# Kernel optimization log

Hardware: AMD Instinct MI355X
Metric: run time of the kernel (lower is better)

## Reference

```python
import jax, jax.numpy as jnp
import numpy as np

B, C, H, W = 32, 384, 32, 32
NCH = 4           # chunks per branch (mixing_size = [4,4,4])
CH = C // NCH     # 96 channels per chunk


def setup_inputs() -> dict:
    key = jax.random.key(0)
    ks = iter(jax.random.split(key, 32))
    r = lambda shape, s=0.05: jax.random.normal(next(ks), shape, dtype=jnp.float32) * s
    inp = {"x": jax.random.normal(next(ks), (B, C, H, W), dtype=jnp.float32)}
    for b, k in zip((1, 2, 3), (1, 3, 5)):
        inp[f"f{b}_mlp_w1"] = r((2, CH, CH // 8))
        inp[f"f{b}_mlp_b1"] = r((2, CH // 8))
        inp[f"f{b}_mlp_w2"] = r((2, CH // 8, CH))
        inp[f"f{b}_mlp_b2"] = r((2, CH))
        inp[f"f{b}_conv_w"] = r((2, CH, 1, k, k))
        inp[f"f{b}_conv_b"] = r((2, CH))
    inp["fusion_w1"] = r((C, C // 4))
    inp["fusion_b1"] = r((C // 4,))
    inp["fusion_w2"] = r((C // 4, 3 * C))
    inp["fusion_b2"] = r((3 * C,))
    inp["proj_w"] = r((C, C))
    inp["proj_b"] = r((C,))
    return inp


def _gelu(x):
    return jax.nn.gelu(x, approximate=False)  # torch nn.GELU default (erf)


def _branch(x, mw1, mb1, mw2, mb2, cw, cb, pad):
    # x: (B, C, H, W); chunks of CH channels; even idx -> MLP (channel-last), odd -> depthwise conv
    chunks = jnp.split(x, NCH, axis=1)
    outs, mi, ci = [], 0, 0
    for i, c in enumerate(chunks):
        if i % 2 == 0:
            h = _gelu(jnp.einsum('bchw,cd->bdhw', c, mw1[mi]) + mb1[mi][:, None, None])
            y = jnp.einsum('bdhw,dc->bchw', h, mw2[mi]) + mb2[mi][:, None, None]
            mi += 1
        else:
            y = jax.lax.conv_general_dilated(
                c, cw[ci], window_strides=(1, 1), padding=[(pad, pad), (pad, pad)],
                feature_group_count=CH, dimension_numbers=('NCHW', 'OIHW', 'NCHW'))
            y = y + cb[ci][:, None, None]
            ci += 1
        outs.append(y)
    return jnp.concatenate(outs, axis=1)


def reference(x,
              f1_mlp_w1, f1_mlp_b1, f1_mlp_w2, f1_mlp_b2, f1_conv_w, f1_conv_b,
              f2_mlp_w1, f2_mlp_b1, f2_mlp_w2, f2_mlp_b2, f2_conv_w, f2_conv_b,
              f3_mlp_w1, f3_mlp_b1, f3_mlp_w2, f3_mlp_b2, f3_conv_w, f3_conv_b,
              fusion_w1, fusion_b1, fusion_w2, fusion_b2, proj_w, proj_b):
    x1 = _branch(x, f1_mlp_w1, f1_mlp_b1, f1_mlp_w2, f1_mlp_b2, f1_conv_w, f1_conv_b, pad=0)
    x2 = _branch(x, f2_mlp_w1, f2_mlp_b1, f2_mlp_w2, f2_mlp_b2, f2_conv_w, f2_conv_b, pad=1)
    x3 = _branch(x, f3_mlp_w1, f3_mlp_b1, f3_mlp_w2, f3_mlp_b2, f3_conv_w, f3_conv_b, pad=2)
    # softmax-gated multi-scale fusion
    a = (x1 + x2 + x3).mean(axis=(2, 3))                            # (B, C)
    g = _gelu(a @ fusion_w1 + fusion_b1) @ fusion_w2 + fusion_b2     # (B, 3C)
    g = g.reshape(a.shape[0], C, 3).transpose(2, 0, 1)               # (3, B, C)
    w = jax.nn.softmax(g, axis=0)[:, :, :, None, None]               # (3, B, C, 1, 1)
    comb = x1 * w[0] + x2 * w[1] + x3 * w[2]                         # (B, C, H, W)
    out = jnp.einsum('bchw,cd->bdhw', comb, proj_w) + proj_b[:, None, None]
    return out
```

## Files before the change

kernel.cpp:

```cpp
#include <hip/hip_runtime.h>
#include <math.h>

#define B_  32
#define C_  384
#define HW  1024

typedef float          f32x4 __attribute__((ext_vector_type(4)));
typedef short          s16x8 __attribute__((ext_vector_type(8)));
typedef unsigned short us8v  __attribute__((ext_vector_type(8)));

#define SWZ(pix) ((((pix) ^ ((pix) >> 4)) & 15) << 4)

struct KParams {
  const float* x;
  const float* mw1[3]; const float* mb1[3]; const float* mw2[3]; const float* mb2[3];
  const float* cw[3];  const float* cb[3];
  const float* fw1; const float* fb1; const float* fw2; const float* fb2;
  const float* pw;  const float* pb;
  float* wg;
  float* H_part;
  float* cvS;
  float* ext;
  unsigned short* pwT;
  unsigned short* hl;
  float* out;
};

__device__ __forceinline__ float gelu_exact(float v) {
  return 0.5f * v * (1.0f + erff(v * 0.70710678118654752440f));
}
__device__ __forceinline__ unsigned short f2bf(float f) {
  unsigned u = __float_as_uint(f);
  u += 0x7FFFu + ((u >> 16) & 1u);
  return (unsigned short)(u >> 16);
}
__device__ __forceinline__ float bf2f(unsigned short h) {
  return __uint_as_float(((unsigned)h) << 16);
}

template<int HALF>
__device__ __forceinline__ void conv_strip(const float* xc, int h0, int row,
                                           float w1t, const float* w3, const float* w5,
                                           float* y0, float* y1, float* y2) {
#pragma unroll
  for (int p = 0; p < 16; ++p) { y0[p] = 0.f; y1[p] = 0.f; y2[p] = 0.f; }
#pragma unroll
  for (int dy = 0; dy < 5; ++dy) {
    const int hr = h0 + row - 2 + dy;
    float win[20];
    if (hr >= 0 && hr < 32) {
#pragma unroll
      for (int u = 0; u < 5; ++u)
        *(float4*)&win[u*4] = *(const float4*)&xc[hr*32 + HALF*12 + u*4];
    } else {
#pragma unroll
      for (int u = 0; u < 20; ++u) win[u] = 0.f;
    }
#pragma unroll
    for (int dx = 0; dx < 5; ++dx) {
      const float w = w5[dy*5 + dx];
#pragma unroll
      for (int p = 0; p < 16; ++p) {
        const int ri = p + dx - 2 + HALF*4;
        if (ri >= 0 && ri < 20) y2[p] += win[ri] * w;
      }
    }
    if (dy >= 1 && dy <= 3) {
#pragma unroll
      for (int dx = 0; dx < 3; ++dx) {
        const float w = w3[(dy-1)*3 + dx];
#pragma unroll
        for (int p = 0; p < 16; ++p) {
          const int ri = p + dx - 1 + HALF*4;
          if (ri >= 0 && ri < 20) y1[p] += win[ri] * w;
        }
      }
      if (dy == 2) {
#pragma unroll
        for (int p = 0; p < 16; ++p) y0[p] = win[p + HALF*4] * w1t;
      }
    }
  }
}

__global__ __launch_bounds__(256, 2) void k_work(KParams P) {
  __shared__ __align__(16) char sm[49152 + 13824 + 256];
  const int bid = blockIdx.x;
  const int t = threadIdx.x;

  if (bid >= 1024) {
    const int pbk = bid - 1024;
    float (*tile)[33] = (float(*)[33])sm;
    const int td = pbk % 12, tc = pbk / 12;
    const int j = t & 31, i0 = t >> 5;
    const int gcoff = (tc < 3) ? 0 : (tc < 6 ? 96 : (tc < 9 ? -96 : 0));
    for (int i = i0; i < 32; i += 8)
      tile[i][j] = P.pw[(size_t)(tc*32 + i + gcoff)*C_ + td*32 + j];
    __syncthreads();
    for (int i = i0; i < 32; i += 8)
      P.pwT[(size_t)(td*32 + i)*C_ + tc*32 + j] = f2bf(tile[j][i]);
    return;
  }

  const int b = bid >> 5, sub = bid & 31;
  if (sub < 16) {
    const int mi = sub >> 3, q = sub & 7;
    const int h0 = q * 4;
    float* Xl  = (float*)sm;
    float* w1l = (float*)(sm + 49152);
    float* Hl  = (float*)(sm + 49152 + 13824);
    for (int i = t; i < 3456; i += 256) {
      int s = i / 1152, r = i - s*1152;
      w1l[i] = P.mw1[s][mi*1152 + r];
    }
    for (int i = t*4; i < 12288; i += 1024) {
      int c = i >> 7, pix = i & 127;
      *(float4*)&Xl[i] = *(const float4*)&P.x[(size_t)(b*C_ + mi*192 + c)*HW + h0*32 + pix];
    }
    __syncthreads();
    const int quad = t & 31, sjg = t >> 6;
    const int cq = (t >> 5) & 1;
    const int sj0 = sjg * 9;
    float h[9][4];
#pragma unroll
    for (int u = 0; u < 9; ++u) { h[u][0]=0.f; h[u][1]=0.f; h[u][2]=0.f; h[u][3]=0.f; }
    int wbase[9];
#pragma unroll
    for (int u = 0; u < 9; ++u) {
      int sj = sj0 + u, s = sj / 12, jj = sj % 12;
      wbase[u] = s*1152 + jj;
    }
    for (int c = cq*48; c < cq*48 + 48; ++c) {
      const float4 xv = *(const float4*)&Xl[c*128 + quad*4];
#pragma unroll
      for (int u = 0; u < 9; ++u) {
        const float w = w1l[wbase[u] + c*12];
        h[u][0] += xv.x*w; h[u][1] += xv.y*w; h[u][2] += xv.z*w; h[u][3] += xv.w*w;
      }
    }
#pragma unroll
    for (int u = 0; u < 9; ++u)
#pragma unroll
      for (int p = 0; p < 4; ++p) h[u][p] += __shfl_xor(h[u][p], 32, 64);
    float hs[9];
#pragma unroll
    for (int u = 0; u < 9; ++u) {
      int sj = sj0 + u, s = sj / 12, jj = sj % 12;
      const float bias = P.mb1[s][mi*12 + jj];
      float g[4];
#pragma unroll
      for (int p = 0; p < 4; ++p) g[p] = gelu_exact(h[u][p] + bias);
      if ((t & 63) < 32) {
        uint2 pk;
        pk.x = (unsigned)f2bf(g[0]) | ((unsigned)f2bf(g[1]) << 16);
        pk.y = (unsigned)f2bf(g[2]) | ((unsigned)f2bf(g[3]) << 16);
        *(uint2*)(P.hl + ((size_t)(b*2 + mi)*36 + sj)*1024 + q*128 + quad*4) = pk;
      }
      float sum = g[0] + g[1] + g[2] + g[3];
#pragma unroll
      for (int m = 16; m >= 1; m >>= 1) sum += __shfl_xor(sum, m, 64);
      hs[u] = sum;
    }
    if ((t & 63) == 0) {
#pragma unroll
      for (int u = 0; u < 9; ++u) Hl[sj0 + u] = hs[u];
    }
    __syncthreads();
    if (t < 36) P.H_part[(size_t)((b*2 + mi)*8 + q)*36 + t] = Hl[t];
  } else {
    const int s2 = sub - 16;
    const int gi = s2 >> 3, q = s2 & 7;
    const int h0 = q * 4;
    const int lane = t & 63, wv = t >> 6;
    const int gcbase = (2*gi + 1) * 96;
    for (int i = 0; i < 24; ++i) {
      const int cc = wv*24 + i;
      const float* xc = P.x + (size_t)(b*C_ + gcbase + cc)*HW + h0*32;
      const float2 v = *(const float2*)(xc + 2*lane);
      const float t2 = v.x + v.y;
      float T = t2;
      T += __shfl_xor(T, 1, 64);  T += __shfl_xor(T, 2, 64);
      T += __shfl_xor(T, 4, 64);  T += __shfl_xor(T, 8, 64);
      T += __shfl_xor(T, 16, 64); T += __shfl_xor(T, 32, 64);
      float c0  = ((lane & 15) == 0)  ? v.x : 0.f;
      float c1  = ((lane & 15) == 0)  ? v.y : 0.f;
      float c30 = ((lane & 15) == 15) ? v.x : 0.f;
      float c31 = ((lane & 15) == 15) ? v.y : 0.f;
      c0  += __shfl_xor(c0, 16, 64);  c0  += __shfl_xor(c0, 32, 64);
      c1  += __shfl_xor(c1, 16, 64);  c1  += __shfl_xor(c1, 32, 64);
      c30 += __shfl_xor(c30, 16, 64); c30 += __shfl_xor(c30, 32, 64);
      c31 += __shfl_xor(c31, 16, 64); c31 += __shfl_xor(c31, 32, 64);
      if (lane == 0) {
        float* S = &P.cvS[(((size_t)(b*2 + gi)*8 + q)*5)*96 + cc];
        S[0*96] = T;   S[1*96] = c0;  S[2*96] = c1;
        S[3*96] = c30; S[4*96] = c31;
      }
      if (q == 0 || q == 7) {
        float r = t2;
        r += __shfl_xor(r, 1, 64); r += __shfl_xor(r, 2, 64);
        r += __shfl_xor(r, 4, 64); r += __shfl_xor(r, 8, 64);
        const int e  = (q == 0) ? 0 : 1;
        const int lo = (q == 0) ? 0 : 32;
        const float Ra  = __shfl(r,   lo,      64), Rb  = __shfl(r,   lo + 16, 64);
        const float p00 = __shfl(v.x, lo,      64), p01 = __shfl(v.y, lo,      64);
        const float p0a = __shfl(v.x, lo + 15, 64), p0b = __shfl(v.y, lo + 15, 64);
        const float p10 = __shfl(v.x, lo + 16, 64), p11 = __shfl(v.y, lo + 16, 64);
        const float p1a = __shfl(v.x, lo + 31, 64), p1b = __shfl(v.y, lo + 31, 64);
        if (lane == 0) {
          float* E = &P.ext[((size_t)(b*2 + gi)*2 + e)*10*96 + cc];
          E[0*96] = Ra;  E[1*96] = Rb;
          E[2*96] = p00; E[3*96] = p01; E[4*96] = p0a; E[5*96] = p0b;
          E[6*96] = p10; E[7*96] = p11; E[8*96] = p1a; E[9*96] = p1b;
        }
      }
    }
  }
}

__global__ __launch_bounds__(512) void k_gate(KParams P) {
  const int b = blockIdx.x, t = threadIdx.x;
  __shared__ float am[C_], g1p[4][96], g1v[96], Hs[2][36];
  for (int i = t; i < 72; i += 512) {
    int mi = i / 36, sj = i % 36;
    float s = 0.f;
    for (int q = 0; q < 8; ++q) s += P.H_part[(size_t)((b*2+mi)*8 + q)*36 + sj];
    Hs[mi][sj] = s * (1.0f/1024.0f);
  }
  __syncthreads();
  if (t < 192) {
    const int mi = t / 96, cc = t % 96;
    float a = 0.f;
    for (int s = 0; s < 3; ++s) {
      float y = P.mb2[s][mi*96 + cc];
      for (int jj = 0; jj < 12; ++jj) y += Hs[mi][s*12+jj] * P.mw2[s][mi*1152 + jj*96 + cc];
      a += y;
    }
    am[mi*192 + cc] = a;
  } else if (t < 384) {
    const int i = t - 192;
    const int gi = i / 96, cc = i % 96;
    const float* S0 = &P.cvS[(((size_t)(b*2 + gi)*8)*5)*96 + cc];
    float T = 0.f, C0 = 0.f, C1 = 0.f, C30 = 0.f, C31 = 0.f;
#pragma unroll
    for (int q = 0; q < 8; ++q) {
      const float* Sq = S0 + (size_t)q*5*96;
      T += Sq[0*96]; C0 += Sq[1*96]; C1 += Sq[2*96]; C30 += Sq[3*96]; C31 += Sq[4*96];
    }
    const float* E0 = &P.ext[((size_t)(b*2 + gi)*2 + 0)*10*96 + cc];
    const float* E1 = &P.ext[((size_t)(b*2 + gi)*2 + 1)*10*96 + cc];
    const float R0  = E0[0*96], R1  = E0[1*96];
    const float a00 = E0[2*96], a01 = E0[3*96], a0a = E0[4*96], a0b = E0[5*96];
    const float a10 = E0[6*96], a11 = E0[7*96], a1a = E0[8*96], a1b = E0[9*96];
    const float R30 = E1[0*96], R31 = E1[1*96];
    const float b00 = E1[2*96], b01 = E1[3*96], b0a = E1[4*96], b0b = E1[5*96];
    const float b10 = E1[6*96], b11 = E1[7*96], b1a = E1[8*96], b1b = E1[9*96];
    const float ER[5]   = {R30+R31, R31, 0.f, R0, R0+R1};
    const float EC[5]   = {C30+C31, C31, 0.f, C0, C0+C1};
    const float cr0[5]  = {a0a+a0b, a0b, 0.f, a00, a00+a01};
    const float cr1[5]  = {a1a+a1b, a1b, 0.f, a10, a10+a11};
    const float cr30[5] = {b0a+b0b, b0b, 0.f, b00, b00+b01};
    const float cr31[5] = {b1a+b1b, b1b, 0.f, b10, b10+b11};
    const int gcl = gi*96 + cc;
    float sum = P.cw[0][gcl] * T;
#pragma unroll
    for (int dy = 0; dy < 3; ++dy)
#pragma unroll
      for (int dx = 0; dx < 3; ++dx) {
        const int s = dy - 1, u = dx - 1;
        float xc_ = 0.f;
        if (s == 1)  xc_ = cr0[u+2];
        if (s == -1) xc_ = cr31[u+2];
        sum += P.cw[1][gcl*9 + dy*3 + dx] * (T - ER[s+2] - EC[u+2] + xc_);
      }
#pragma unroll
    for (int dy = 0; dy < 5; ++dy)
#pragma unroll
      for (int dx = 0; dx < 5; ++dx) {
        const int s = dy - 2, u = dx - 2;
        float xc_ = 0.f;
        if (s == 1)  xc_ = cr0[u+2];
        if (s == 2)  xc_ = cr0[u+2] + cr1[u+2];
        if (s == -1) xc_ = cr31[u+2];
        if (s == -2) xc_ = cr30[u+2] + cr31[u+2];
        sum += P.cw[2][gcl*25 + dy*5 + dx] * (T - ER[s+2] - EC[u+2] + xc_);
      }
    am[(2*gi+1)*96 + cc] = sum * (1.0f/1024.0f)
                         + P.cb[0][gcl] + P.cb[1][gcl] + P.cb[2][gcl];
  }
  __syncthreads();
  if (t < 384) {
    const int quarter = t / 96, jj = t % 96;
    float acc = 0.f;
    for (int c = quarter*96; c < quarter*96 + 96; ++c) acc += am[c] * P.fw1[c*96 + jj];
    g1p[quarter][jj] = acc;
  }
  __syncthreads();
  if (t < 96) g1v[t] = gelu_exact(g1p[0][t] + g1p[1][t] + g1p[2][t] + g1p[3][t] + P.fb1[t]);
  __syncthreads();
  if (t < 384) {
    const int c = t;
    float l0 = P.fb2[c*3+0], l1 = P.fb2[c*3+1], l2 = P.fb2[c*3+2];
    for (int jj = 0; jj < 96; ++jj) {
      const float g = g1v[jj];
      const float* f = P.fw2 + jj*1152 + c*3;
      l0 += g*f[0]; l1 += g*f[1]; l2 += g*f[2];
    }
    const float m = fmaxf(l0, fmaxf(l1, l2));
    const float e0 = expf(l0-m), e1 = expf(l1-m), e2 = expf(l2-m);
    const float inv = 1.0f/(e0+e1+e2);
    P.wg[0*(B_*C_) + b*C_ + c] = e0*inv;
    P.wg[1*(B_*C_) + b*C_ + c] = e1*inv;
    P.wg[2*(B_*C_) + b*C_ + c] = e2*inv;
  }
}

__global__ __launch_bounds__(512, 1) void k_proj(KParams P) {
  __shared__ __align__(16) char smem[135168];
  char* combB = smem;
  char* hlB   = smem + 98304;
  unsigned short* wlB = (unsigned short*)(smem + 117120);
  float* wgl  = (float*)(smem + 130944);

  const int t  = threadIdx.x;
  const int rb = (blockIdx.x & 7) * 32 + (blockIdx.x >> 3);
  const int b  = rb >> 3;
  const int qv = rb & 7;
  const int h0 = qv * 4;

  for (int i = t; i < 1152; i += 512)
    wgl[i] = P.wg[(size_t)(i/C_)*(B_*C_) + b*C_ + (i % C_)];
  for (int i = t; i < 6912; i += 512) {
    int s = i / 2304, r = i - s*2304;
    wlB[i] = f2bf(P.mw2[s][r]);
  }
  for (int i = t; i < 2304; i += 512) {
    const int sjmi = i >> 5, pg = i & 31;
    const uint2 v = *(const uint2*)(P.hl + ((size_t)(b*72 + sjmi))*1024 + qv*128 + pg*4);
    *(uint2*)(hlB + sjmi*256 + pg*8) = v;
  }
  __syncthreads();

  for (int it = 0; it < 3; ++it) {
    const int tt = t + 512*it;
    const int hlf = (tt >= 768) ? 1 : 0;
    const int rem = tt - hlf*768;
    const int row = rem & 3, c192 = rem >> 2;
    const int gi = c192 / 96, cc = c192 - gi*96;
    const int gcl = gi*96 + cc;
    const int gc = (2*gi + 1)*96 + cc;
    const int kp = 192 + gi*96 + cc;
    const float* xc = P.x + (size_t)(b*C_ + gc)*HW;
    const float w1t = P.cw[0][gcl];
    float w3[9], w5[25];
#pragma unroll
    for (int k2 = 0; k2 < 9; ++k2)  w3[k2] = P.cw[1][gcl*9 + k2];
#pragma unroll
    for (int k2 = 0; k2 < 25; ++k2) w5[k2] = P.cw[2][gcl*25 + k2];
    float y0[16], y1[16], y2[16];
    if (hlf == 0) conv_strip<0>(xc, h0, row, w1t, w3, w5, y0, y1, y2);
    else          conv_strip<1>(xc, h0, row, w1t, w3, w5, y0, y1, y2);
    const float g0 = wgl[0*C_ + gc], g1 = wgl[1*C_ + gc], g2 = wgl[2*C_ + gc];
    const float cbg = g0*P.cb[0][gcl] + g1*P.cb[1][gcl] + g2*P.cb[2][gcl];
#pragma unroll
    for (int p = 0; p < 16; ++p) {
      const float v = g0*y0[p] + g1*y1[p] + g2*y2[p] + cbg;
      const int pix = row*32 + hlf*16 + p;
      const int off = pix*768 + ((kp*2) ^ SWZ(pix));
      *(unsigned short*)(combB + off) = f2bf(v);
    }
  }

  {
    const int ct = t & 15, pt = (t >> 4) & 15, mi = t >> 8;
    const int c0 = ct*6, pix0 = pt*8;
    float wgc[3][6];
#pragma unroll
    for (int s = 0; s < 3; ++s)
#pragma unroll
      for (int i = 0; i < 6; ++i) wgc[s][i] = wgl[s*C_ + mi*192 + c0 + i];
    float acc[6][8];
#pragma unroll
    for (int i = 0; i < 6; ++i) {
      float ai = 0.f;
#pragma unroll
      for (int s = 0; s < 3; ++s) ai += wgc[s][i] * P.mb2[s][mi*96 + c0 + i];
#pragma unroll
      for (int p = 0; p < 8; ++p) acc[i][p] = ai;
    }
#pragma unroll
    for (int s = 0; s < 3; ++s)
#pragma unroll
      for (int jj = 0; jj < 12; ++jj) {
        const us8v hv = *(const us8v*)(hlB + (mi*36 + s*12 + jj)*256 + pix0*2);
        float hf[8];
#pragma unroll
        for (int p = 0; p < 8; ++p) hf[p] = bf2f(hv[p]);
        const unsigned short* wp = wlB + (s*2 + mi)*1152 + jj*96 + c0;
        float gw[6];
#pragma unroll
        for (int i = 0; i < 6; ++i) gw[i] = bf2f(wp[i]) * wgc[s][i];
#pragma unroll
        for (int i = 0; i < 6; ++i)
#pragma unroll
          for (int p = 0; p < 8; ++p) acc[i][p] += gw[i]*hf[p];
      }
#pragma unroll
    for (int i = 0; i < 6; ++i)
#pragma unroll
      for (int p = 0; p < 8; ++p) {
        const int pix = pix0 + p;
        const int kp2 = mi*96 + c0 + i;
        const int off = pix*768 + ((kp2*2) ^ SWZ(pix));
        *(unsigned short*)(combB + off) = f2bf(acc[i][p]);
      }
  }
  __syncthreads();

  {
    const int lane = t & 63, wv = t >> 6;
    const int wm = wv & 1, wn = wv >> 1;
    const int l15 = lane & 15, l4 = lane >> 4;
    f32x4 acc[4][6];
#pragma unroll
    for (int mt = 0; mt < 4; ++mt)
#pragma unroll
      for (int nt = 0; nt < 6; ++nt) acc[mt][nt] = (f32x4){0.f,0.f,0.f,0.f};
    const char* pwTb = (const char*)P.pwT;
#pragma unroll 2
    for (int ks = 0; ks < 12; ++ks) {
      const int k0 = ks*32 + l4*8;
      s16x8 af[4], bfr[6];
#pragma unroll
      for (int mt = 0; mt < 4; ++mt) {
        const int m = wm*64 + mt*16 + l15;
        af[mt] = *(const s16x8*)(combB + m*768 + ((2*k0) ^ SWZ(m)));
      }
#pragma unroll
      for (int nt = 0; nt < 6; ++nt) {
        const int d = wn*96 + nt*16 + l15;
        bfr[nt] = *(const s16x8*)(pwTb + (size_t)d*768 + 2*k0);
      }
#pragma unroll
      for (int mt = 0; mt < 4; ++mt)
#pragma unroll
        for (int nt = 0; nt < 6; ++nt)
          acc[mt][nt] = __builtin_amdgcn_mfma_f32_16x16x32_bf16(af[mt], bfr[nt], acc[mt][nt], 0, 0, 0);
    }
#pragma unroll
    for (int nt = 0; nt < 6; ++nt) {
      const int d = wn*96 + nt*16 + l15;
      const float pbv = P.pb[d];
#pragma unroll
      for (int mt = 0; mt < 4; ++mt) {
        const int pix = wm*64 + mt*16 + l4*4;
        float4 o;
        o.x = acc[mt][nt][0] + pbv;
        o.y = acc[mt][nt][1] + pbv;
        o.z = acc[mt][nt][2] + pbv;
        o.w = acc[mt][nt][3] + pbv;
        *(float4*)&P.out[(size_t)(b*C_ + d)*HW + (h0 + (pix >> 5))*32 + (pix & 31)] = o;
      }
    }
  }
}

extern "C" void kernel_launch(void* const* d_in, const int* in_sizes, int n_in,
                              void* d_out, int out_size, void* d_ws, size_t ws_size,
                              hipStream_t stream) {
  KParams P;
  P.x = (const float*)d_in[0];
  for (int s = 0; s < 3; ++s) {
    const int base = 1 + s * 6;
    P.mw1[s] = (const float*)d_in[base + 0];
    P.mb1[s] = (const float*)d_in[base + 1];
    P.mw2[s] = (const float*)d_in[base + 2];
    P.mb2[s] = (const float*)d_in[base + 3];
    P.cw[s]  = (const float*)d_in[base + 4];
    P.cb[s]  = (const float*)d_in[base + 5];
  }
  P.fw1 = (const float*)d_in[19]; P.fb1 = (const float*)d_in[20];
  P.fw2 = (const float*)d_in[21]; P.fb2 = (const float*)d_in[22];
  P.pw  = (const float*)d_in[23]; P.pb  = (const float*)d_in[24];
  float* w = (float*)d_ws;
  P.wg     = w;
  P.H_part = w + 36864;
  P.cvS    = w + 55296;
  P.ext    = w + 301056;
  P.pwT    = (unsigned short*)(w + 423936);
  P.hl     = (unsigned short*)(w + 497664);
  P.out = (float*)d_out;

  k_work<<<1168, 256, 0, stream>>>(P);
  k_gate<<<32, 512, 0, stream>>>(P);
  k_proj<<<256, 512, 0, stream>>>(P);
}
```

Before: 248.2 us.

## Split work kernel into MLP and aux kernels; halve proj tile rows

The fused k_work kernel becomes two kernels. k_mlp handles the first-layer MLP blocks, and k_aux handles the conv-statistics and proj-weight transpose blocks, so the small blocks no longer reserve the large shared-memory footprint. k_proj now processes 2 image rows per block instead of 4, which doubles the grid to 512 blocks and cuts shared memory from about 132KB to 75KB. The intent is better occupancy and more parallelism in the dominant kernel. The cost is an extra launch, and each proj-weight fragment is reused across fewer pixel rows, so loads of pwT from global/L2 double.

```diff
diff --git a/kernel.cpp b/kernel.cpp
--- a/kernel.cpp
+++ b/kernel.cpp
@@ -83,14 +83,82 @@
   }
 }
 
-__global__ __launch_bounds__(256, 2) void k_work(KParams P) {
+__global__ __launch_bounds__(256, 2) void k_mlp(KParams P) {
   __shared__ __align__(16) char sm[49152 + 13824 + 256];
   const int bid = blockIdx.x;
   const int t = threadIdx.x;
-
-  if (bid >= 1024) {
-    const int pbk = bid - 1024;
-    float (*tile)[33] = (float(*)[33])sm;
+  const int b = bid >> 4, mi = (bid >> 3) & 1, q = bid & 7;
+  const int h0 = q * 4;
+  float* Xl  = (float*)sm;
+  float* w1l = (float*)(sm + 49152);
+  float* Hl  = (float*)(sm + 49152 + 13824);
+  for (int i = t; i < 3456; i += 256) {
+    int s = i / 1152, r = i - s*1152;
+    w1l[i] = P.mw1[s][mi*1152 + r];
+  }
+  for (int i = t*4; i < 12288; i += 1024) {
+    int c = i >> 7, pix = i & 127;
+    *(float4*)&Xl[i] = *(const float4*)&P.x[(size_t)(b*C_ + mi*192 + c)*HW + h0*32 + pix];
+  }
+  __syncthreads();
+  const int quad = t & 31, sjg = t >> 6;
+  const int cq = (t >> 5) & 1;
+  const int sj0 = sjg * 9;
+  float h[9][4];
+#pragma unroll
+  for (int u = 0; u < 9; ++u) { h[u][0]=0.f; h[u][1]=0.f; h[u][2]=0.f; h[u][3]=0.f; }
+  int wbase[9];
+#pragma unroll
+  for (int u = 0; u < 9; ++u) {
+    int sj = sj0 + u, s = sj / 12, jj = sj % 12;
+    wbase[u] = s*1152 + jj;
+  }
+  for (int c = cq*48; c < cq*48 + 48; ++c) {
+    const float4 xv = *(const float4*)&Xl[c*128 + quad*4];
+#pragma unroll
+    for (int u = 0; u < 9; ++u) {
+      const float w = w1l[wbase[u] + c*12];
+      h[u][0] += xv.x*w; h[u][1] += xv.y*w; h[u][2] += xv.z*w; h[u][3] += xv.w*w;
+    }
+  }
+#pragma unroll
+  for (int u = 0; u < 9; ++u)
+#pragma unroll
+    for (int p = 0; p < 4; ++p) h[u][p] += __shfl_xor(h[u][p], 32, 64);
+  float hs[9];
+#pragma unroll
+  for (int u = 0; u < 9; ++u) {
+    int sj = sj0 + u, s = sj / 12, jj = sj % 12;
+    const float bias = P.mb1[s][mi*12 + jj];
+    float g[4];
+#pragma unroll
+    for (int p = 0; p < 4; ++p) g[p] = gelu_exact(h[u][p] + bias);
+    if ((t & 63) < 32) {
+      uint2 pk;
+      pk.x = (unsigned)f2bf(g[0]) | ((unsigned)f2bf(g[1]) << 16);
+      pk.y = (unsigned)f2bf(g[2]) | ((unsigned)f2bf(g[3]) << 16);
+      *(uint2*)(P.hl + ((size_t)(b*2 + mi)*36 + sj)*1024 + q*128 + quad*4) = pk;
+    }
+    float sum = g[0] + g[1] + g[2] + g[3];
+#pragma unroll
+    for (int m = 16; m >= 1; m >>= 1) sum += __shfl_xor(sum, m, 64);
+    hs[u] = sum;
+  }
+  if ((t & 63) == 0) {
+#pragma unroll
+    for (int u = 0; u < 9; ++u) Hl[sj0 + u] = hs[u];
+  }
+  __syncthreads();
+  if (t < 36) P.H_part[(size_t)((b*2 + mi)*8 + q)*36 + t] = Hl[t];
+}
+
+__global__ __launch_bounds__(256, 2) void k_aux(KParams P) {
+  __shared__ float tile[32][33];
+  const int bid = blockIdx.x;
+  const int t = threadIdx.x;
+
+  if (bid >= 512) {
+    const int pbk = bid - 512;
     const int td = pbk % 12, tc = pbk / 12;
     const int j = t & 31, i0 = t >> 5;
     const int gcoff = (tc < 3) ? 0 : (tc < 6 ? 96 : (tc < 9 ? -96 : 0));
@@ -102,116 +170,49 @@
     return;
   }
 
-  const int b = bid >> 5, sub = bid & 31;
-  if (sub < 16) {
-    const int mi = sub >> 3, q = sub & 7;
-    const int h0 = q * 4;
-    float* Xl  = (float*)sm;
-    float* w1l = (float*)(sm + 49152);
-    float* Hl  = (float*)(sm + 49152 + 13824);
-    for (int i = t; i < 3456; i += 256) {
-      int s = i / 1152, r = i - s*1152;
-      w1l[i] = P.mw1[s][mi*1152 + r];
-    }
-    for (int i = t*4; i < 12288; i += 1024) {
-      int c = i >> 7, pix = i & 127;
-      *(float4*)&Xl[i] = *(const float4*)&P.x[(size_t)(b*C_ + mi*192 + c)*HW + h0*32 + pix];
-    }
-    __syncthreads();
-    const int quad = t & 31, sjg = t >> 6;
-    const int cq = (t >> 5) & 1;
-    const int sj0 = sjg * 9;
-    float h[9][4];
-#pragma unroll
-    for (int u = 0; u < 9; ++u) { h[u][0]=0.f; h[u][1]=0.f; h[u][2]=0.f; h[u][3]=0.f; }
-    int wbase[9];
-#pragma unroll
-    for (int u = 0; u < 9; ++u) {
-      int sj = sj0 + u, s = sj / 12, jj = sj % 12;
-      wbase[u] = s*1152 + jj;
-    }
-    for (int c = cq*48; c < cq*48 + 48; ++c) {
-      const float4 xv = *(const float4*)&Xl[c*128 + quad*4];
-#pragma unroll
-      for (int u = 0; u < 9; ++u) {
-        const float w = w1l[wbase[u] + c*12];
-        h[u][0] += xv.x*w; h[u][1] += xv.y*w; h[u][2] += xv.z*w; h[u][3] += xv.w*w;
-      }
-    }
-#pragma unroll
-    for (int u = 0; u < 9; ++u)
-#pragma unroll
-      for (int p = 0; p < 4; ++p) h[u][p] += __shfl_xor(h[u][p], 32, 64);
-    float hs[9];
-#pragma unroll
-    for (int u = 0; u < 9; ++u) {
-      int sj = sj0 + u, s = sj / 12, jj = sj % 12;
-      const float bias = P.mb1[s][mi*12 + jj];
-      float g[4];
-#pragma unroll
-      for (int p = 0; p < 4; ++p) g[p] = gelu_exact(h[u][p] + bias);
-      if ((t & 63) < 32) {
-        uint2 pk;
-        pk.x = (unsigned)f2bf(g[0]) | ((unsigned)f2bf(g[1]) << 16);
-        pk.y = (unsigned)f2bf(g[2]) | ((unsigned)f2bf(g[3]) << 16);
-        *(uint2*)(P.hl + ((size_t)(b*2 + mi)*36 + sj)*1024 + q*128 + quad*4) = pk;
-      }
-      float sum = g[0] + g[1] + g[2] + g[3];
-#pragma unroll
-      for (int m = 16; m >= 1; m >>= 1) sum += __shfl_xor(sum, m, 64);
-      hs[u] = sum;
-    }
-    if ((t & 63) == 0) {
-#pragma unroll
-      for (int u = 0; u < 9; ++u) Hl[sj0 + u] = hs[u];
-    }
-    __syncthreads();
-    if (t < 36) P.H_part[(size_t)((b*2 + mi)*8 + q)*36 + t] = Hl[t];
-  } else {
-    const int s2 = sub - 16;
-    const int gi = s2 >> 3, q = s2 & 7;
-    const int h0 = q * 4;
-    const int lane = t & 63, wv = t >> 6;
-    const int gcbase = (2*gi + 1) * 96;
-    for (int i = 0; i < 24; ++i) {
-      const int cc = wv*24 + i;
-      const float* xc = P.x + (size_t)(b*C_ + gcbase + cc)*HW + h0*32;
-      const float2 v = *(const float2*)(xc + 2*lane);
-      const float t2 = v.x + v.y;
-      float T = t2;
-      T += __shfl_xor(T, 1, 64);  T += __shfl_xor(T, 2, 64);
-      T += __shfl_xor(T, 4, 64);  T += __shfl_xor(T, 8, 64);
-      T += __shfl_xor(T, 16, 64); T += __shfl_xor(T, 32, 64);
-      float c0  = ((lane & 15) == 0)  ? v.x : 0.f;
-      float c1  = ((lane & 15) == 0)  ? v.y : 0.f;
-      float c30 = ((lane & 15) == 15) ? v.x : 0.f;
-      float c31 = ((lane & 15) == 15) ? v.y : 0.f;
-      c0  += __shfl_xor(c0, 16, 64);  c0  += __shfl_xor(c0, 32, 64);
-      c1  += __shfl_xor(c1, 16, 64);  c1  += __shfl_xor(c1, 32, 64);
-      c30 += __shfl_xor(c30, 16, 64); c30 += __shfl_xor(c30, 32, 64);
-      c31 += __shfl_xor(c31, 16, 64); c31 += __shfl_xor(c31, 32, 64);
+  const int b = bid >> 4, s2 = bid & 15;
+  const int gi = s2 >> 3, q = s2 & 7;
+  const int h0 = q * 4;
+  const int lane = t & 63, wv = t >> 6;
+  const int gcbase = (2*gi + 1) * 96;
+  for (int i = 0; i < 24; ++i) {
+    const int cc = wv*24 + i;
+    const float* xc = P.x + (size_t)(b*C_ + gcbase + cc)*HW + h0*32;
+    const float2 v = *(const float2*)(xc + 2*lane);
+    const float t2 = v.x + v.y;
+    float T = t2;
+    T += __shfl_xor(T, 1, 64);  T += __shfl_xor(T, 2, 64);
+    T += __shfl_xor(T, 4, 64);  T += __shfl_xor(T, 8, 64);
+    T += __shfl_xor(T, 16, 64); T += __shfl_xor(T, 32, 64);
+    float c0  = ((lane & 15) == 0)  ? v.x : 0.f;
+    float c1  = ((lane & 15) == 0)  ? v.y : 0.f;
+    float c30 = ((lane & 15) == 15) ? v.x : 0.f;
+    float c31 = ((lane & 15) == 15) ? v.y : 0.f;
+    c0  += __shfl_xor(c0, 16, 64);  c0  += __shfl_xor(c0, 32, 64);
+    c1  += __shfl_xor(c1, 16, 64);  c1  += __shfl_xor(c1, 32, 64);
+    c30 += __shfl_xor(c30, 16, 64); c30 += __shfl_xor(c30, 32, 64);
+    c31 += __shfl_xor(c31, 16, 64); c31 += __shfl_xor(c31, 32, 64);
+    if (lane == 0) {
+      float* S = &P.cvS[(((size_t)(b*2 + gi)*8 + q)*5)*96 + cc];
+      S[0*96] = T;   S[1*96] = c0;  S[2*96] = c1;
+      S[3*96] = c30; S[4*96] = c31;
+    }
+    if (q == 0 || q == 7) {
+      float r = t2;
+      r += __shfl_xor(r, 1, 64); r += __shfl_xor(r, 2, 64);
+      r += __shfl_xor(r, 4, 64); r += __shfl_xor(r, 8, 64);
+      const int e  = (q == 0) ? 0 : 1;
+      const int lo = (q == 0) ? 0 : 32;
+      const float Ra  = __shfl(r,   lo,      64), Rb  = __shfl(r,   lo + 16, 64);
+      const float p00 = __shfl(v.x, lo,      64), p01 = __shfl(v.y, lo,      64);
+      const float p0a = __shfl(v.x, lo + 15, 64), p0b = __shfl(v.y, lo + 15, 64);
+      const float p10 = __shfl(v.x, lo + 16, 64), p11 = __shfl(v.y, lo + 16, 64);
+      const float p1a = __shfl(v.x, lo + 31, 64), p1b = __shfl(v.y, lo + 31, 64);
       if (lane == 0) {
-        float* S = &P.cvS[(((size_t)(b*2 + gi)*8 + q)*5)*96 + cc];
-        S[0*96] = T;   S[1*96] = c0;  S[2*96] = c1;
-        S[3*96] = c30; S[4*96] = c31;
-      }
-      if (q == 0 || q == 7) {
-        float r = t2;
-        r += __shfl_xor(r, 1, 64); r += __shfl_xor(r, 2, 64);
-        r += __shfl_xor(r, 4, 64); r += __shfl_xor(r, 8, 64);
-        const int e  = (q == 0) ? 0 : 1;
-        const int lo = (q == 0) ? 0 : 32;
-        const float Ra  = __shfl(r,   lo,      64), Rb  = __shfl(r,   lo + 16, 64);
-        const float p00 = __shfl(v.x, lo,      64), p01 = __shfl(v.y, lo,      64);
-        const float p0a = __shfl(v.x, lo + 15, 64), p0b = __shfl(v.y, lo + 15, 64);
-        const float p10 = __shfl(v.x, lo + 16, 64), p11 = __shfl(v.y, lo + 16, 64);
-        const float p1a = __shfl(v.x, lo + 31, 64), p1b = __shfl(v.y, lo + 31, 64);
-        if (lane == 0) {
-          float* E = &P.ext[((size_t)(b*2 + gi)*2 + e)*10*96 + cc];
-          E[0*96] = Ra;  E[1*96] = Rb;
-          E[2*96] = p00; E[3*96] = p01; E[4*96] = p0a; E[5*96] = p0b;
-          E[6*96] = p10; E[7*96] = p11; E[8*96] = p1a; E[9*96] = p1b;
-        }
+        float* E = &P.ext[((size_t)(b*2 + gi)*2 + e)*10*96 + cc];
+        E[0*96] = Ra;  E[1*96] = Rb;
+        E[2*96] = p00; E[3*96] = p01; E[4*96] = p0a; E[5*96] = p0b;
+        E[6*96] = p10; E[7*96] = p11; E[8*96] = p1a; E[9*96] = p1b;
       }
     }
   }
@@ -315,17 +316,17 @@
 }
 
 __global__ __launch_bounds__(512, 1) void k_proj(KParams P) {
-  __shared__ __align__(16) char smem[135168];
+  __shared__ __align__(16) char smem[76800];
   char* combB = smem;
-  char* hlB   = smem + 98304;
-  unsigned short* wlB = (unsigned short*)(smem + 117120);
-  float* wgl  = (float*)(smem + 130944);
+  char* hlB   = smem + 49152;
+  unsigned short* wlB = (unsigned short*)(smem + 58368);
+  float* wgl  = (float*)(smem + 72192);
 
   const int t  = threadIdx.x;
-  const int rb = (blockIdx.x & 7) * 32 + (blockIdx.x >> 3);
-  const int b  = rb >> 3;
-  const int qv = rb & 7;
-  const int h0 = qv * 4;
+  const int rb = (blockIdx.x & 7) * 64 + (blockIdx.x >> 3);
+  const int b  = rb >> 4;
+  const int tq = rb & 15;
+  const int h0 = tq * 2;
 
   for (int i = t; i < 1152; i += 512)
     wgl[i] = P.wg[(size_t)(i/C_)*(B_*C_) + b*C_ + (i % C_)];
@@ -333,54 +334,56 @@
     int s = i / 2304, r = i - s*2304;
     wlB[i] = f2bf(P.mw2[s][r]);
   }
-  for (int i = t; i < 2304; i += 512) {
-    const int sjmi = i >> 5, pg = i & 31;
-    const uint2 v = *(const uint2*)(P.hl + ((size_t)(b*72 + sjmi))*1024 + qv*128 + pg*4);
-    *(uint2*)(hlB + sjmi*256 + pg*8) = v;
-  }
-  __syncthreads();
-
-  for (int it = 0; it < 3; ++it) {
-    const int tt = t + 512*it;
-    const int hlf = (tt >= 768) ? 1 : 0;
-    const int rem = tt - hlf*768;
-    const int row = rem & 3, c192 = rem >> 2;
-    const int gi = c192 / 96, cc = c192 - gi*96;
-    const int gcl = gi*96 + cc;
-    const int gc = (2*gi + 1)*96 + cc;
-    const int kp = 192 + gi*96 + cc;
-    const float* xc = P.x + (size_t)(b*C_ + gc)*HW;
-    const float w1t = P.cw[0][gcl];
-    float w3[9], w5[25];
-#pragma unroll
-    for (int k2 = 0; k2 < 9; ++k2)  w3[k2] = P.cw[1][gcl*9 + k2];
-#pragma unroll
-    for (int k2 = 0; k2 < 25; ++k2) w5[k2] = P.cw[2][gcl*25 + k2];
-    float y0[16], y1[16], y2[16];
-    if (hlf == 0) conv_strip<0>(xc, h0, row, w1t, w3, w5, y0, y1, y2);
-    else          conv_strip<1>(xc, h0, row, w1t, w3, w5, y0, y1, y2);
-    const float g0 = wgl[0*C_ + gc], g1 = wgl[1*C_ + gc], g2 = wgl[2*C_ + gc];
-    const float cbg = g0*P.cb[0][gcl] + g1*P.cb[1][gcl] + g2*P.cb[2][gcl];
-#pragma unroll
-    for (int p = 0; p < 16; ++p) {
-      const float v = g0*y0[p] + g1*y1[p] + g2*y2[p] + cbg;
-      const int pix = row*32 + hlf*16 + p;
-      const int off = pix*768 + ((kp*2) ^ SWZ(pix));
-      *(unsigned short*)(combB + off) = f2bf(v);
+  for (int i = t; i < 1152; i += 512) {
+    const int sjmi = i >> 4, pg = i & 15;
+    const uint2 v = *(const uint2*)(P.hl + ((size_t)(b*72 + sjmi))*1024 + tq*64 + pg*4);
+    *(uint2*)(hlB + sjmi*128 + pg*8) = v;
+  }
+  __syncthreads();
+
+  for (int it = 0; it < 2; ++it) {
+    const int task = t + 512*it;
+    if (task < 768) {
+      const int hlf = (task >= 384) ? 1 : 0;
+      const int rem = task - hlf*384;
+      const int row = rem & 1, c192 = rem >> 1;
+      const int gi = c192 / 96, cc = c192 - gi*96;
+      const int gcl = gi*96 + cc;
+      const int gc = (2*gi + 1)*96 + cc;
+      const int kp = 192 + gi*96 + cc;
+      const float* xc = P.x + (size_t)(b*C_ + gc)*HW;
+      const float w1t = P.cw[0][gcl];
+      float w3[9], w5[25];
+#pragma unroll
+      for (int k2 = 0; k2 < 9; ++k2)  w3[k2] = P.cw[1][gcl*9 + k2];
+#pragma unroll
+      for (int k2 = 0; k2 < 25; ++k2) w5[k2] = P.cw[2][gcl*25 + k2];
+      float y0[16], y1[16], y2[16];
+      if (hlf == 0) conv_strip<0>(xc, h0, row, w1t, w3, w5, y0, y1, y2);
+      else          conv_strip<1>(xc, h0, row, w1t, w3, w5, y0, y1, y2);
+      const float g0 = wgl[0*C_ + gc], g1 = wgl[1*C_ + gc], g2 = wgl[2*C_ + gc];
+      const float cbg = g0*P.cb[0][gcl] + g1*P.cb[1][gcl] + g2*P.cb[2][gcl];
+#pragma unroll
+      for (int p = 0; p < 16; ++p) {
+        const float v = g0*y0[p] + g1*y1[p] + g2*y2[p] + cbg;
+        const int pix = row*32 + hlf*16 + p;
+        const int off = pix*768 + ((kp*2) ^ SWZ(pix));
+        *(unsigned short*)(combB + off) = f2bf(v);
+      }
     }
   }
 
   {
-    const int ct = t & 15, pt = (t >> 4) & 15, mi = t >> 8;
-    const int c0 = ct*6, pix0 = pt*8;
-    float wgc[3][6];
+    const int ct = t & 31, pt = (t >> 5) & 7, mi = t >> 8;
+    const int c0 = ct*3, pix0 = pt*8;
+    float wgc[3][3];
 #pragma unroll
     for (int s = 0; s < 3; ++s)
 #pragma unroll
-      for (int i = 0; i < 6; ++i) wgc[s][i] = wgl[s*C_ + mi*192 + c0 + i];
-    float acc[6][8];
-#pragma unroll
-    for (int i = 0; i < 6; ++i) {
+      for (int i = 0; i < 3; ++i) wgc[s][i] = wgl[s*C_ + mi*192 + c0 + i];
+    float acc[3][8];
+#pragma unroll
+    for (int i = 0; i < 3; ++i) {
       float ai = 0.f;
 #pragma unroll
       for (int s = 0; s < 3; ++s) ai += wgc[s][i] * P.mb2[s][mi*96 + c0 + i];
@@ -391,21 +394,21 @@
     for (int s = 0; s < 3; ++s)
 #pragma unroll
       for (int jj = 0; jj < 12; ++jj) {
-        const us8v hv = *(const us8v*)(hlB + (mi*36 + s*12 + jj)*256 + pix0*2);
+        const us8v hv = *(const us8v*)(hlB + (mi*36 + s*12 + jj)*128 + pix0*2);
         float hf[8];
 #pragma unroll
         for (int p = 0; p < 8; ++p) hf[p] = bf2f(hv[p]);
         const unsigned short* wp = wlB + (s*2 + mi)*1152 + jj*96 + c0;
-        float gw[6];
-#pragma unroll
-        for (int i = 0; i < 6; ++i) gw[i] = bf2f(wp[i]) * wgc[s][i];
-#pragma unroll
-        for (int i = 0; i < 6; ++i)
+        float gw[3];
+#pragma unroll
+        for (int i = 0; i < 3; ++i) gw[i] = bf2f(wp[i]) * wgc[s][i];
+#pragma unroll
+        for (int i = 0; i < 3; ++i)
 #pragma unroll
           for (int p = 0; p < 8; ++p) acc[i][p] += gw[i]*hf[p];
       }
 #pragma unroll
-    for (int i = 0; i < 6; ++i)
+    for (int i = 0; i < 3; ++i)
 #pragma unroll
       for (int p = 0; p < 8; ++p) {
         const int pix = pix0 + p;
@@ -420,19 +423,19 @@
     const int lane = t & 63, wv = t >> 6;
     const int wm = wv & 1, wn = wv >> 1;
     const int l15 = lane & 15, l4 = lane >> 4;
-    f32x4 acc[4][6];
-#pragma unroll
-    for (int mt = 0; mt < 4; ++mt)
+    f32x4 acc[2][6];
+#pragma unroll
+    for (int mt = 0; mt < 2; ++mt)
 #pragma unroll
       for (int nt = 0; nt < 6; ++nt) acc[mt][nt] = (f32x4){0.f,0.f,0.f,0.f};
     const char* pwTb = (const char*)P.pwT;
 #pragma unroll 2
     for (int ks = 0; ks < 12; ++ks) {
       const int k0 = ks*32 + l4*8;
-      s16x8 af[4], bfr[6];
-#pragma unroll
-      for (int mt = 0; mt < 4; ++mt) {
-        const int m = wm*64 + mt*16 + l15;
+      s16x8 af[2], bfr[6];
+#pragma unroll
+      for (int mt = 0; mt < 2; ++mt) {
+        const int m = wm*32 + mt*16 + l15;
         af[mt] = *(const s16x8*)(combB + m*768 + ((2*k0) ^ SWZ(m)));
       }
 #pragma unroll
@@ -441,7 +444,7 @@
         bfr[nt] = *(const s16x8*)(pwTb + (size_t)d*768 + 2*k0);
       }
 #pragma unroll
-      for (int mt = 0; mt < 4; ++mt)
+      for (int mt = 0; mt < 2; ++mt)
 #pragma unroll
         for (int nt = 0; nt < 6; ++nt)
           acc[mt][nt] = __builtin_amdgcn_mfma_f32_16x16x32_bf16(af[mt], bfr[nt], acc[mt][nt], 0, 0, 0);
@@ -451,14 +454,14 @@
       const int d = wn*96 + nt*16 + l15;
       const float pbv = P.pb[d];
 #pragma unroll
-      for (int mt = 0; mt < 4; ++mt) {
-        const int pix = wm*64 + mt*16 + l4*4;
+      for (int mt = 0; mt < 2; ++mt) {
+        const int pix = wm*32 + mt*16 + l4*4;
         float4 o;
         o.x = acc[mt][nt][0] + pbv;
         o.y = acc[mt][nt][1] + pbv;
         o.z = acc[mt][nt][2] + pbv;
         o.w = acc[mt][nt][3] + pbv;
-        *(float4*)&P.out[(size_t)(b*C_ + d)*HW + (h0 + (pix >> 5))*32 + (pix & 31)] = o;
+        *(float4*)&P.out[(size_t)(b*C_ + d)*HW + tq*64 + pix] = o;
       }
     }
   }
@@ -490,7 +493,8 @@
   P.hl     = (unsigned short*)(w + 497664);
   P.out = (float*)d_out;
 
-  k_work<<<1168, 256, 0, stream>>>(P);
+  k_mlp <<<512, 256, 0, stream>>>(P);
+  k_aux <<<656, 256, 0, stream>>>(P);
   k_gate<<<32, 512, 0, stream>>>(P);
-  k_proj<<<256, 512, 0, stream>>>(P);
-}
+  k_proj<<<512, 512, 0, stream>>>(P);
+}
```

After: 273.7 us. 1.1x slower.
